# Optimization experiments

Measured on AMD Instinct MI355X. Metric: run time of the kernel, lower is better.

Reference implementation:

```python
import jax, jax.numpy as jnp
import numpy as np

B, L, D, H = 2, 2048, 1024, 16
DH = D // H  # per-head dim = 64


def setup_inputs() -> dict:
    key = jax.random.key(0)
    ks = jax.random.split(key, 7)
    s = 1.0 / np.sqrt(D)
    x = jax.random.normal(ks[0], (B, L, D), dtype=jnp.float32)
    Wq = jax.random.normal(ks[1], (D, D), dtype=jnp.float32) * s
    bq = jax.random.normal(ks[2], (D,), dtype=jnp.float32) * s
    Wk = jax.random.normal(ks[3], (D, D), dtype=jnp.float32) * s
    bk = jax.random.normal(ks[4], (D,), dtype=jnp.float32) * s
    Wv = jax.random.normal(ks[5], (D, D), dtype=jnp.float32) * s
    bv = jax.random.normal(ks[6], (D,), dtype=jnp.float32) * s
    # strict upper-triangular causal mask; mask==1 means position is masked (-inf)
    atten_mask = jnp.triu(jnp.ones((L, L), dtype=jnp.int32), k=1)
    return {"x": x, "atten_mask": atten_mask, "Wq": Wq, "bq": bq,
            "Wk": Wk, "bk": bk, "Wv": Wv, "bv": bv}


def reference(x, atten_mask, Wq, bq, Wk, bk, Wv, bv):
    # nn.Linear: y = x @ W^T + b
    q = x @ Wq.T + bq  # [B,L,D]
    k = x @ Wk.T + bk
    v = x @ Wv.T + bv
    # contiguous split into heads == reshape to [B,L,H,DH]
    q = q.reshape(B, L, H, DH)
    k = k.reshape(B, L, H, DH)
    v = v.reshape(B, L, H, DH)
    scale = jnp.sqrt(jnp.float32(DH))
    scores = jnp.einsum('blhd,bmhd->bhlm', q, k) / scale  # [B,H,L,L]
    # torch.where(mask == 1, -inf, scores)
    scores = jnp.where(atten_mask[None, None] == 1, -jnp.inf, scores)
    attn = jax.nn.softmax(scores, axis=-1)
    out = jnp.einsum('bhlm,bmhd->blhd', attn, v)  # [B,L,H,DH]
    return out.reshape(B, L, D)  # concat heads along channel dim
```

## Files before the change

### kernel.cpp

```cpp
#include <hip/hip_runtime.h>
#include <hip/hip_bf16.h>

#define BDIM 2
#define LSEQ 2048
#define DMODEL 1024
#define NH 16
#define DHEAD 64
#define SP 40
#define RST 68
#define CTS 136

typedef __bf16 bf16_t;
typedef __attribute__((ext_vector_type(8))) __bf16 bf16x8;
typedef __attribute__((ext_vector_type(4))) __bf16 bf16x4;
typedef __attribute__((ext_vector_type(2))) __bf16 bf16x2;
typedef __attribute__((ext_vector_type(4))) float f32x4;
typedef __attribute__((ext_vector_type(4))) int i32x4;

static __device__ __forceinline__ f32x4 mfma16(bf16x8 a, bf16x8 b, f32x4 c) {
    return __builtin_amdgcn_mfma_f32_16x16x32_bf16(a, b, c, 0, 0, 0);
}

static __device__ __forceinline__ void load_lds16(const bf16_t* g, void* l) {
    __builtin_amdgcn_global_load_lds(
        (const __attribute__((address_space(1))) void*)g,
        (__attribute__((address_space(3))) void*)l, 16, 0, 0);
}

__global__ void convert_all(
    const float* __restrict__ x,
    const float* __restrict__ Wq, const float* __restrict__ Wk, const float* __restrict__ Wv,
    const float* __restrict__ bq, const float* __restrict__ bk, const float* __restrict__ bv,
    bf16_t* __restrict__ cx,
    bf16_t* __restrict__ cWq, bf16_t* __restrict__ cWk, bf16_t* __restrict__ cWv,
    bf16_t* __restrict__ cbq, bf16_t* __restrict__ cbk, bf16_t* __restrict__ cbv,
    float SQ)
{
    const int blk = blockIdx.x;
    const float* src; bf16_t* dst; int base, cnt; float sc = 1.0f;
    if (blk < 1024)      { src = x;  dst = cx;  base = blk * 1024;          cnt = 1024; }
    else if (blk < 1280) { src = Wq; dst = cWq; base = (blk - 1024) * 1024; cnt = 1024; sc = SQ; }
    else if (blk < 1536) { src = Wk; dst = cWk; base = (blk - 1280) * 1024; cnt = 1024; }
    else if (blk < 1792) { src = Wv; dst = cWv; base = (blk - 1536) * 1024; cnt = 1024; }
    else if (blk == 1792){ src = bq; dst = cbq; base = 0; cnt = 256; sc = SQ; }
    else if (blk == 1793){ src = bk; dst = cbk; base = 0; cnt = 256; }
    else                 { src = bv; dst = cbv; base = 0; cnt = 256; }

    for (int i = base + threadIdx.x; i < base + cnt; i += 256) {
        f32x4 v = *(const f32x4*)(src + 4 * (size_t)i);
        bf16x4 o;
        o[0] = (bf16_t)(v[0] * sc); o[1] = (bf16_t)(v[1] * sc);
        o[2] = (bf16_t)(v[2] * sc); o[3] = (bf16_t)(v[3] * sc);
        *(bf16x4*)(dst + 4 * (size_t)i) = o;
    }
}

__global__ __launch_bounds__(512, 2) void qkv_gemm(
    const bf16_t* __restrict__ x,
    const bf16_t* __restrict__ W0, const bf16_t* __restrict__ W1, const bf16_t* __restrict__ W2,
    const bf16_t* __restrict__ b0, const bf16_t* __restrict__ b1, const bf16_t* __restrict__ b2,
    bf16_t* __restrict__ yq, bf16_t* __restrict__ yk, bf16_t* __restrict__ yvT)
{
    __shared__ alignas(16) bf16_t smem[81920];

    const int tid  = threadIdx.x;
    const int lane = tid & 63;
    const int w    = tid >> 6;
    const int quad = lane >> 4;
    const int n16  = lane & 15;
    const int swz  = n16 & 7;
    const int srow = lane >> 3;
    const int schnk = (lane & 7) ^ srow;

    const int s   = blockIdx.x;
    const int sem = ((s & 7) << 3) | (s >> 3);
    const int m0  = (sem >> 2) * 256;
    const int n0  = (sem & 3) * 256;
    const int z   = blockIdx.y;

    const bf16_t* W    = (z == 0) ? W0 : ((z == 1) ? W1 : W2);
    const bf16_t* bias = (z == 0) ? b0 : ((z == 1) ? b1 : b2);

    const int wm = (w >> 2) * 128;
    const int wn = (w & 3) * 64;

    const bf16_t* gA = x + (size_t)(m0 + w * 8 + srow) * DMODEL + schnk * 8;
    const bf16_t* gB = W + (size_t)(n0 + w * 8 + srow) * DMODEL + schnk * 8;

    f32x4 acc[8][4] = {};

    auto stageA = [&](int abuf, int h, int kt) {
        bf16_t* d = smem + abuf * 16384 + (h * 128 + w * 8) * 64;
        const bf16_t* src = gA + (size_t)(h * 128) * DMODEL + kt * 64;
        load_lds16(src, d);
        load_lds16(src + (size_t)64 * DMODEL, d + 64 * 64);
    };
    auto stageB = [&](int slot, int h, int kt) {
        bf16_t* d = smem + 32768 + slot * 16384 + (h * 128 + w * 8) * 64;
        const bf16_t* src = gB + (size_t)(h * 128) * DMODEL + kt * 64;
        load_lds16(src, d);
        load_lds16(src + (size_t)64 * DMODEL, d + 64 * 64);
    };

    stageA(0, 0, 0); stageA(0, 1, 0);
    stageB(0, 0, 0); stageB(0, 1, 0);
    stageB(1, 0, 1); stageB(1, 1, 1);
    asm volatile("s_waitcnt vmcnt(4)" ::: "memory");
    __builtin_amdgcn_s_barrier();

    int bs = 0;
    for (int u = 0; u < 16; ++u) {
        const int abuf = u & 1;
        const bf16_t* Ab = smem + abuf * 16384;
        const bf16_t* Bb = smem + 32768 + bs * 16384;
        const int bs2 = (bs + 2 >= 3) ? bs - 1 : bs + 2;

        bf16x8 bfr[4][2], aX[2][2], aY[2][2];

        #pragma unroll
        for (int nt = 0; nt < 4; ++nt) {
            const bf16_t* br = Bb + (wn + nt * 16 + n16) * 64;
            bfr[nt][0] = *(const bf16x8*)(br + ((quad    ) ^ swz) * 8);
            bfr[nt][1] = *(const bf16x8*)(br + ((quad + 4) ^ swz) * 8);
        }
        #pragma unroll
        for (int m2 = 0; m2 < 2; ++m2) {
            const bf16_t* ar = Ab + (wm + m2 * 16 + n16) * 64;
            aX[m2][0] = *(const bf16x8*)(ar + ((quad    ) ^ swz) * 8);
            aX[m2][1] = *(const bf16x8*)(ar + ((quad + 4) ^ swz) * 8);
        }
        if (u + 1 < 16) { stageA(abuf ^ 1, 0, u + 1); stageA(abuf ^ 1, 1, u + 1); }
        if (u + 2 < 16) { stageB(bs2, 0, u + 2);      stageB(bs2, 1, u + 2); }

        #pragma unroll
        for (int m2 = 0; m2 < 2; ++m2) {
            const bf16_t* ar = Ab + (wm + (2 + m2) * 16 + n16) * 64;
            aY[m2][0] = *(const bf16x8*)(ar + ((quad    ) ^ swz) * 8);
            aY[m2][1] = *(const bf16x8*)(ar + ((quad + 4) ^ swz) * 8);
        }
        #pragma unroll
        for (int m2 = 0; m2 < 2; ++m2)
            #pragma unroll
            for (int nt = 0; nt < 4; ++nt) {
                acc[m2][nt] = mfma16(aX[m2][0], bfr[nt][0], acc[m2][nt]);
                acc[m2][nt] = mfma16(aX[m2][1], bfr[nt][1], acc[m2][nt]);
            }

        #pragma unroll
        for (int m2 = 0; m2 < 2; ++m2) {
            const bf16_t* ar = Ab + (wm + (4 + m2) * 16 + n16) * 64;
            aX[m2][0] = *(const bf16x8*)(ar + ((quad    ) ^ swz) * 8);
            aX[m2][1] = *(const bf16x8*)(ar + ((quad + 4) ^ swz) * 8);
        }
        #pragma unroll
        for (int m2 = 0; m2 < 2; ++m2)
            #pragma unroll
            for (int nt = 0; nt < 4; ++nt) {
                acc[2 + m2][nt] = mfma16(aY[m2][0], bfr[nt][0], acc[2 + m2][nt]);
                acc[2 + m2][nt] = mfma16(aY[m2][1], bfr[nt][1], acc[2 + m2][nt]);
            }

        #pragma unroll
        for (int m2 = 0; m2 < 2; ++m2) {
            const bf16_t* ar = Ab + (wm + (6 + m2) * 16 + n16) * 64;
            aY[m2][0] = *(const bf16x8*)(ar + ((quad    ) ^ swz) * 8);
            aY[m2][1] = *(const bf16x8*)(ar + ((quad + 4) ^ swz) * 8);
        }
        #pragma unroll
        for (int m2 = 0; m2 < 2; ++m2)
            #pragma unroll
            for (int nt = 0; nt < 4; ++nt) {
                acc[4 + m2][nt] = mfma16(aX[m2][0], bfr[nt][0], acc[4 + m2][nt]);
                acc[4 + m2][nt] = mfma16(aX[m2][1], bfr[nt][1], acc[4 + m2][nt]);
            }

        #pragma unroll
        for (int m2 = 0; m2 < 2; ++m2)
            #pragma unroll
            for (int nt = 0; nt < 4; ++nt) {
                acc[6 + m2][nt] = mfma16(aY[m2][0], bfr[nt][0], acc[6 + m2][nt]);
                acc[6 + m2][nt] = mfma16(aY[m2][1], bfr[nt][1], acc[6 + m2][nt]);
            }

        if (u < 14) asm volatile("s_waitcnt vmcnt(4)" ::: "memory");
        else        asm volatile("s_waitcnt vmcnt(0)" ::: "memory");
        __builtin_amdgcn_s_barrier();
        bs = (bs + 1 == 3) ? 0 : bs + 1;
    }

    if (z < 2) {
        bf16_t* y = (z == 0) ? yq : yk;
        bf16_t* Ct = smem;
        #pragma unroll
        for (int hp = 0; hp < 2; ++hp) {
            if (((w & 3) >> 1) == hp) {
                #pragma unroll
                for (int nt = 0; nt < 4; ++nt) {
                    const int jc = (w & 1) * 64 + nt * 16 + n16;
                    const float bv = (float)bias[n0 + hp * 128 + jc];
                    #pragma unroll
                    for (int mt = 0; mt < 8; ++mt) {
                        const int rr = wm + mt * 16 + quad * 4;
                        #pragma unroll
                        for (int r = 0; r < 4; ++r)
                            Ct[(rr + r) * CTS + jc] = (bf16_t)(acc[mt][nt][r] + bv);
                    }
                }
            }
            __syncthreads();
            const int row = tid >> 1;
            const int seg = tid & 1;
            const int hh  = (n0 >> 6) + hp * 2 + seg;
            const int i   = m0 + row;
            const int bb  = i >> 11, ll = i & 2047;
            bf16_t* dst = &y[(((size_t)bb * NH + hh) * LSEQ + ll) * DHEAD];
            const bf16_t* srcr = &Ct[row * CTS + seg * 64];
            #pragma unroll
            for (int c = 0; c < 8; ++c)
                *(bf16x8*)(dst + c * 8) = *(const bf16x8*)(srcr + c * 8);
            __syncthreads();
        }
    } else {
        #pragma unroll
        for (int nt = 0; nt < 4; ++nt) {
            const int j = n0 + wn + nt * 16 + n16;
            const float bv = (float)bias[j];
            #pragma unroll
            for (int mt = 0; mt < 8; ++mt) {
                const int i0 = m0 + wm + mt * 16 + quad * 4;
                const int bb = i0 >> 11, l = i0 & 2047;
                bf16x4 pk;
                #pragma unroll
                for (int r = 0; r < 4; ++r) pk[r] = (bf16_t)(acc[mt][nt][r] + bv);
                *(bf16x4*)(&yvT[((size_t)bb * DMODEL + j) * LSEQ + l]) = pk;
            }
        }
    }
}

__global__ __launch_bounds__(256, 2) void attn_fused(
    const bf16_t* __restrict__ qp,
    const bf16_t* __restrict__ kp,
    const bf16_t* __restrict__ vtp,
    float* __restrict__ out,
    float* __restrict__ Opart,
    float* __restrict__ ml)
{
    __shared__ alignas(16) char arena[69632];
    float* Rex = (float*)(arena);

    const int tid  = threadIdx.x;
    const int lane = tid & 63;
    const int w    = tid >> 6;
    const int quad = lane >> 4;
    const int n16  = lane & 15;
    const int lane3 = lane >> 3;
    const int lane7 = lane & 7;
    const int swz8  = (lane7 ^ lane3) * 8;
    const int swz   = n16 & 7;

    const int wq   = (w >> 1) * 64;
    const int wkv  = (w & 1) * 32;
    const int pairI = w >> 1;
    const bool isOdd = (w & 1) != 0;
    bf16_t* Pw0 = (bf16_t*)(arena + 49152) + w * (64 * SP);

    const int bh  = blockIdx.x;
    const int yy  = blockIdx.y;
    const int p   = yy & 7;
    const bool isA = (yy < 8);
    const int b = bh >> 4, h = bh & 15;
    const size_t hb = (size_t)bh * (LSEQ * DHEAD);

    float l_[4];
    f32x4 oacc[4][4];

    auto zero_state = [&]() {
        #pragma unroll
        for (int g = 0; g < 4; ++g) {
            l_[g] = 0.f;
            #pragma unroll
            for (int mv = 0; mv < 4; ++mv) { f32x4 zz = {0.f,0.f,0.f,0.f}; oacc[mv][g] = zz; }
        }
    };

    auto process = [&](int qt, int t0, int ntiles, bool maskTail) {
        int iqg[4];
        bf16x8 qb[4][2];
        #pragma unroll
        for (int g = 0; g < 4; ++g) {
            iqg[g] = qt * 128 + wq + 16 * g + n16;
            const bf16_t* qq = qp + hb + (size_t)iqg[g] * DHEAD;
            qb[g][0] = *(const bf16x8*)(qq + quad * 8);
            qb[g][1] = *(const bf16x8*)(qq + 32 + quad * 8);
        }

        const bf16_t* gk0 = kp  + hb + (size_t)(t0 * 64 + 16 * w + lane3) * DHEAD + swz8;
        const bf16_t* gv0 = vtp + hb + (size_t)(16 * w + lane3) * LSEQ + t0 * 64 + swz8;

        auto stageKV = [&](int slot, int it) {
            char* lk = arena + slot * 8192 + w * 2048;
            char* lv = arena + 24576 + slot * 8192 + w * 2048;
            const bf16_t* kK = gk0 + (size_t)it * 64 * DHEAD;
            const bf16_t* vV = gv0 + (size_t)it * 64;
            load_lds16(kK,             lk);
            load_lds16(kK + 8 * DHEAD, lk + 1024);
            load_lds16(vV,             lv);
            load_lds16(vV + 8 * LSEQ,  lv + 1024);
        };

        stageKV(0, 0);
        if (ntiles > 1) { stageKV(1, 1); asm volatile("s_waitcnt vmcnt(4)" ::: "memory"); }
        else            {                asm volatile("s_waitcnt vmcnt(0)" ::: "memory"); }
        __builtin_amdgcn_s_barrier();

        int slot = 0;
        for (int it = 0; it < ntiles; ++it) {
            const int s2 = (slot + 2 >= 3) ? slot - 1 : slot + 2;
            if (it + 2 < ntiles) stageKV(s2, it + 2);

            const bf16_t* kb = (const bf16_t*)(arena + slot * 8192);
            f32x4 s[2][4];
            #pragma unroll
            for (int m = 0; m < 2; ++m) {
                const bf16_t* krow = kb + (wkv + 16 * m + n16) * 64;
                bf16x8 k0v = *(const bf16x8*)(krow + ((quad    ) ^ swz) * 8);
                bf16x8 k1v = *(const bf16x8*)(krow + ((quad + 4) ^ swz) * 8);
                #pragma unroll
                for (int g = 0; g < 4; ++g) {
                    f32x4 z = {0.f, 0.f, 0.f, 0.f};
                    z = mfma16(k0v, qb[g][0], z);
                    z = mfma16(k1v, qb[g][1], z);
                    s[m][g] = z;
                }
            }

            if (maskTail && it >= ntiles - 2) {
                const int k0 = (t0 + it) * 64 + wkv;
                #pragma unroll
                for (int m = 0; m < 2; ++m)
                    #pragma unroll
                    for (int g = 0; g < 4; ++g)
                        #pragma unroll
                        for (int r = 0; r < 4; ++r)
                            if (k0 + 16 * m + quad * 4 + r > iqg[g]) s[m][g][r] = -1e30f;
            }

            #pragma unroll
            for (int g = 0; g < 4; ++g) {
                float rs = 0.f;
                #pragma unroll
                for (int m = 0; m < 2; ++m) {
                    float p0 = __builtin_amdgcn_exp2f(s[m][g][0]);
                    float p1 = __builtin_amdgcn_exp2f(s[m][g][1]);
                    float p2 = __builtin_amdgcn_exp2f(s[m][g][2]);
                    float p3 = __builtin_amdgcn_exp2f(s[m][g][3]);
                    rs += (p0 + p1) + (p2 + p3);
                    bf16x4 pk;
                    pk[0] = (bf16_t)p0; pk[1] = (bf16_t)p1;
                    pk[2] = (bf16_t)p2; pk[3] = (bf16_t)p3;
                    *(bf16x4*)(Pw0 + (16 * g + n16) * SP + 16 * m + quad * 4) = pk;
                }
                l_[g] += rs;
            }

            asm volatile("s_waitcnt lgkmcnt(0)" ::: "memory");

            const bf16_t* vb = (const bf16_t*)(arena + 24576 + slot * 8192);
            bf16x8 pb[4];
            #pragma unroll
            for (int g = 0; g < 4; ++g)
                pb[g] = *(const bf16x8*)(Pw0 + (16 * g + n16) * SP + quad * 8);
            #pragma unroll
            for (int mv = 0; mv < 4; ++mv) {
                const bf16_t* vrow = vb + (16 * mv + n16) * 64;
                bf16x8 va = *(const bf16x8*)(vrow + ((((w & 1) * 4) + quad) ^ swz) * 8);
                #pragma unroll
                for (int g = 0; g < 4; ++g)
                    oacc[mv][g] = mfma16(va, pb[g], oacc[mv][g]);
            }

            if (it + 2 < ntiles) asm volatile("s_waitcnt vmcnt(4)" ::: "memory");
            else                 asm volatile("s_waitcnt vmcnt(0)" ::: "memory");
            __builtin_amdgcn_s_barrier();
            slot = (slot + 1 == 3) ? 0 : slot + 1;
        }
    };

    auto reduce_pair = [&]() {
        __syncthreads();
        float* Rb = Rex + pairI * (64 * RST);
        if (isOdd) {
            #pragma unroll
            for (int g = 0; g < 4; ++g) {
                #pragma unroll
                for (int mv = 0; mv < 4; ++mv)
                    *(f32x4*)(Rb + (16 * g + n16) * RST + 16 * mv + quad * 4) = oacc[mv][g];
                Rb[(16 * g + n16) * RST + 64 + quad] = l_[g];
            }
        }
        __syncthreads();
        if (!isOdd) {
            #pragma unroll
            for (int g = 0; g < 4; ++g) {
                #pragma unroll
                for (int mv = 0; mv < 4; ++mv) {
                    f32x4 t = *(const f32x4*)(Rb + (16 * g + n16) * RST + 16 * mv + quad * 4);
                    oacc[mv][g][0] += t[0]; oacc[mv][g][1] += t[1];
                    oacc[mv][g][2] += t[2]; oacc[mv][g][3] += t[3];
                }
                float ls = l_[g] + Rb[(16 * g + n16) * RST + 64 + quad];
                ls += __shfl_xor(ls, 16, 64);
                ls += __shfl_xor(ls, 32, 64);
                l_[g] = ls;
            }
        }
        __syncthreads();
    };

    auto store_partial = [&](int pidx) {
        if (isOdd) return;
        #pragma unroll
        for (int g = 0; g < 4; ++g) {
            const int row = wq + 16 * g + n16;
            float* Ob = Opart + (size_t)pidx * (128 * 64) + row * 64;
            #pragma unroll
            for (int mv = 0; mv < 4; ++mv)
                *(f32x4*)(Ob + 16 * mv + quad * 4) = oacc[mv][g];
            if (quad == 0) ml[(size_t)pidx * 128 + row] = l_[g];
        }
    };

    if (isA) {
        zero_state();
        process(p, 0, 2 * p + 2, true);
        reduce_pair();
        if (!isOdd) {
            #pragma unroll
            for (int g = 0; g < 4; ++g) {
                const float inv = 1.0f / l_[g];
                const int iq = p * 128 + wq + 16 * g + n16;
                float* orow = out + ((size_t)b * LSEQ + iq) * DMODEL + h * DHEAD;
                #pragma unroll
                for (int mv = 0; mv < 4; ++mv) {
                    f32x4 o;
                    o[0] = oacc[mv][g][0] * inv; o[1] = oacc[mv][g][1] * inv;
                    o[2] = oacc[mv][g][2] * inv; o[3] = oacc[mv][g][3] * inv;
                    *(f32x4*)(orow + 16 * mv + quad * 4) = o;
                }
            }
        }
        zero_state();
        process(15 - p, 0, 15 - 2 * p, false);
        reduce_pair();
        store_partial((bh * 8 + (7 - p)) * 2 + 0);
    } else {
        zero_state();
        process(15 - p, 15 - 2 * p, 17, true);
        reduce_pair();
        store_partial((bh * 8 + (7 - p)) * 2 + 1);
    }
}

__global__ __launch_bounds__(256) void attn_combine(
    const float* __restrict__ Opart, const float* __restrict__ ml,
    float* __restrict__ out)
{
    const int bh = blockIdx.x;
    const int q8 = blockIdx.y;
    const int t  = threadIdx.x;
    const int row = t >> 1;
    const int dh0 = (t & 1) * 32;
    const int p0  = (bh * 8 + q8) * 2;
    const int b = bh >> 4, h = bh & 15;

    float l0 = ml[(size_t)p0 * 128 + row];
    float l1 = ml[(size_t)(p0 + 1) * 128 + row];
    float inv = 1.0f / (l0 + l1);

    const float* P0 = Opart + (size_t)p0 * (128 * 64) + row * 64 + dh0;
    const float* P1 = P0 + 128 * 64;
    float* orow = out + ((size_t)b * LSEQ + ((8 + q8) * 128 + row)) * DMODEL
                + h * DHEAD + dh0;
    #pragma unroll
    for (int c = 0; c < 8; ++c) {
        f32x4 o0 = *(const f32x4*)(P0 + 4 * c);
        f32x4 o1 = *(const f32x4*)(P1 + 4 * c);
        f32x4 o;
        o[0] = (o0[0] + o1[0]) * inv;
        o[1] = (o0[1] + o1[1]) * inv;
        o[2] = (o0[2] + o1[2]) * inv;
        o[3] = (o0[3] + o1[3]) * inv;
        *(f32x4*)(orow + 4 * c) = o;
    }
}

extern "C" void kernel_launch(void* const* d_in, const int* in_sizes, int n_in,
                              void* d_out, int out_size, void* d_ws, size_t ws_size,
                              hipStream_t stream)
{
    const float* x  = (const float*)d_in[0];
    const float* Wq = (const float*)d_in[2];
    const float* bq = (const float*)d_in[3];
    const float* Wk = (const float*)d_in[4];
    const float* bk = (const float*)d_in[5];
    const float* Wv = (const float*)d_in[6];
    const float* bv = (const float*)d_in[7];
    float* out = (float*)d_out;

    char* ws = (char*)d_ws;
    bf16_t* q   = (bf16_t*)(ws);
    bf16_t* k   = (bf16_t*)(ws + 8u  * 1024 * 1024);
    bf16_t* vT  = (bf16_t*)(ws + 16u * 1024 * 1024);
    bf16_t* cx  = (bf16_t*)(ws + 24u * 1024 * 1024);
    bf16_t* cWq = (bf16_t*)(ws + 32u * 1024 * 1024);
    bf16_t* cWk = (bf16_t*)(ws + 34u * 1024 * 1024);
    bf16_t* cWv = (bf16_t*)(ws + 36u * 1024 * 1024);
    bf16_t* cbq = (bf16_t*)(ws + 38u * 1024 * 1024);
    bf16_t* cbk = (bf16_t*)(ws + 38u * 1024 * 1024 + 4096);
    bf16_t* cbv = (bf16_t*)(ws + 38u * 1024 * 1024 + 8192);
    float*  mlp = (float*) (ws + 39u * 1024 * 1024);
    float*  Op  = (float*) (ws + 40u * 1024 * 1024);

    const float SQ = 0.125f * 1.44269504088896f;

    convert_all<<<1795, 256, 0, stream>>>(x, Wq, Wk, Wv, bq, bk, bv,
                                          cx, cWq, cWk, cWv, cbq, cbk, cbv, SQ);

    dim3 g1(64, 3, 1);
    qkv_gemm<<<g1, 512, 0, stream>>>(cx, cWq, cWk, cWv, cbq, cbk, cbv, q, k, vT);

    dim3 g2(BDIM * NH, 16, 1);
    attn_fused<<<g2, 256, 0, stream>>>(q, k, vT, out, Op, mlp);

    dim3 g3(BDIM * NH, 8, 1);
    attn_combine<<<g3, 256, 0, stream>>>(Op, mlp, out);
}
```

Before: 167.3 us.

## Shrink QKV GEMM to 128x128 tiles with simple double-buffered pipeline

Replaces the 256x256 tile, 512-thread QKV projection GEMM (triple-buffered B, double-buffered A, interleaved fragment loads, swizzled block order) with a 128x128 tile, 256-thread kernel using plain double buffering and __syncthreads. The grid grows from 192 to 768 blocks, which improves occupancy and load balance across CUs. In exchange, operand reuse per block drops and global/L2 traffic rises. The finer-grained prefetch/barrier scheduling is also lost.

Measured after the change: 168.9 us. No clear change (+0.9%).

```diff
diff --git a/kernel.cpp b/kernel.cpp
--- a/kernel.cpp
+++ b/kernel.cpp
@@ -55,180 +55,125 @@
     }
 }
 
-__global__ __launch_bounds__(512, 2) void qkv_gemm(
+__global__ __launch_bounds__(256) void qkv_gemm(
     const bf16_t* __restrict__ x,
     const bf16_t* __restrict__ W0, const bf16_t* __restrict__ W1, const bf16_t* __restrict__ W2,
     const bf16_t* __restrict__ b0, const bf16_t* __restrict__ b1, const bf16_t* __restrict__ b2,
     bf16_t* __restrict__ yq, bf16_t* __restrict__ yk, bf16_t* __restrict__ yvT)
 {
-    __shared__ alignas(16) bf16_t smem[81920];
+    __shared__ alignas(16) bf16_t smem[2 * 16384];
+    bf16_t* Ct = smem;
 
     const int tid  = threadIdx.x;
     const int lane = tid & 63;
     const int w    = tid >> 6;
     const int quad = lane >> 4;
     const int n16  = lane & 15;
-    const int swz  = n16 & 7;
-    const int srow = lane >> 3;
-    const int schnk = (lane & 7) ^ srow;
-
-    const int s   = blockIdx.x;
-    const int sem = ((s & 7) << 3) | (s >> 3);
-    const int m0  = (sem >> 2) * 256;
-    const int n0  = (sem & 3) * 256;
-    const int z   = blockIdx.y;
+
+    const int m0 = blockIdx.y * 128;
+    const int n0 = blockIdx.x * 128;
+    const int z  = blockIdx.z;
 
     const bf16_t* W    = (z == 0) ? W0 : ((z == 1) ? W1 : W2);
     const bf16_t* bias = (z == 0) ? b0 : ((z == 1) ? b1 : b2);
 
-    const int wm = (w >> 2) * 128;
-    const int wn = (w & 3) * 64;
-
-    const bf16_t* gA = x + (size_t)(m0 + w * 8 + srow) * DMODEL + schnk * 8;
-    const bf16_t* gB = W + (size_t)(n0 + w * 8 + srow) * DMODEL + schnk * 8;
-
-    f32x4 acc[8][4] = {};
-
-    auto stageA = [&](int abuf, int h, int kt) {
-        bf16_t* d = smem + abuf * 16384 + (h * 128 + w * 8) * 64;
-        const bf16_t* src = gA + (size_t)(h * 128) * DMODEL + kt * 64;
-        load_lds16(src, d);
-        load_lds16(src + (size_t)64 * DMODEL, d + 64 * 64);
-    };
-    auto stageB = [&](int slot, int h, int kt) {
-        bf16_t* d = smem + 32768 + slot * 16384 + (h * 128 + w * 8) * 64;
-        const bf16_t* src = gB + (size_t)(h * 128) * DMODEL + kt * 64;
-        load_lds16(src, d);
-        load_lds16(src + (size_t)64 * DMODEL, d + 64 * 64);
-    };
-
-    stageA(0, 0, 0); stageA(0, 1, 0);
-    stageB(0, 0, 0); stageB(0, 1, 0);
-    stageB(1, 0, 1); stageB(1, 1, 1);
-    asm volatile("s_waitcnt vmcnt(4)" ::: "memory");
-    __builtin_amdgcn_s_barrier();
-
-    int bs = 0;
-    for (int u = 0; u < 16; ++u) {
-        const int abuf = u & 1;
-        const bf16_t* Ab = smem + abuf * 16384;
-        const bf16_t* Bb = smem + 32768 + bs * 16384;
-        const int bs2 = (bs + 2 >= 3) ? bs - 1 : bs + 2;
-
-        bf16x8 bfr[4][2], aX[2][2], aY[2][2];
-
-        #pragma unroll
-        for (int nt = 0; nt < 4; ++nt) {
-            const bf16_t* br = Bb + (wn + nt * 16 + n16) * 64;
-            bfr[nt][0] = *(const bf16x8*)(br + ((quad    ) ^ swz) * 8);
-            bfr[nt][1] = *(const bf16x8*)(br + ((quad + 4) ^ swz) * 8);
-        }
-        #pragma unroll
-        for (int m2 = 0; m2 < 2; ++m2) {
-            const bf16_t* ar = Ab + (wm + m2 * 16 + n16) * 64;
-            aX[m2][0] = *(const bf16x8*)(ar + ((quad    ) ^ swz) * 8);
-            aX[m2][1] = *(const bf16x8*)(ar + ((quad + 4) ^ swz) * 8);
-        }
-        if (u + 1 < 16) { stageA(abuf ^ 1, 0, u + 1); stageA(abuf ^ 1, 1, u + 1); }
-        if (u + 2 < 16) { stageB(bs2, 0, u + 2);      stageB(bs2, 1, u + 2); }
-
-        #pragma unroll
-        for (int m2 = 0; m2 < 2; ++m2) {
-            const bf16_t* ar = Ab + (wm + (2 + m2) * 16 + n16) * 64;
-            aY[m2][0] = *(const bf16x8*)(ar + ((quad    ) ^ swz) * 8);
-            aY[m2][1] = *(const bf16x8*)(ar + ((quad + 4) ^ swz) * 8);
-        }
-        #pragma unroll
-        for (int m2 = 0; m2 < 2; ++m2)
+    const int wm = (w >> 1) * 64;
+    const int wn = (w & 1) * 64;
+
+    f32x4 acc[4][4] = {};
+
+    const int srow  = lane >> 3;
+    const int schnk = (lane & 7) ^ srow;
+    const bf16_t* gx = x + (size_t)(m0 + w * 32 + srow) * DMODEL + schnk * 8;
+    const bf16_t* gw = W + (size_t)(n0 + w * 32 + srow) * DMODEL + schnk * 8;
+    const int dOff = w * 2048;
+
+    const int swz = n16 & 7;
+
+    {
+        bf16_t* lA = smem + dOff;
+        bf16_t* lB = smem + 8192 + dOff;
+        #pragma unroll
+        for (int ii = 0; ii < 4; ++ii) {
+            load_lds16(gx + (size_t)(8 * ii) * DMODEL, lA + ii * 512);
+            load_lds16(gw + (size_t)(8 * ii) * DMODEL, lB + ii * 512);
+        }
+    }
+    __syncthreads();
+
+    int buf = 0;
+    for (int it = 0; it < 16; ++it) {
+        if (it + 1 < 16) {
+            const int k0 = (it + 1) * 64;
+            bf16_t* lA = smem + (buf ^ 1) * 16384 + dOff;
+            bf16_t* lB = smem + (buf ^ 1) * 16384 + 8192 + dOff;
+            #pragma unroll
+            for (int ii = 0; ii < 4; ++ii) {
+                load_lds16(gx + (size_t)(8 * ii) * DMODEL + k0, lA + ii * 512);
+                load_lds16(gw + (size_t)(8 * ii) * DMODEL + k0, lB + ii * 512);
+            }
+        }
+
+        const bf16_t* Ab = smem + buf * 16384;
+        const bf16_t* Bb = smem + buf * 16384 + 8192;
+        #pragma unroll
+        for (int kk = 0; kk < 2; ++kk) {
+            bf16x8 af[4], bfv[4];
+            #pragma unroll
+            for (int mt = 0; mt < 4; ++mt) {
+                const bf16_t* ar = Ab + (wm + mt * 16 + n16) * 64;
+                af[mt] = *(const bf16x8*)(ar + ((quad + 4 * kk) ^ swz) * 8);
+            }
             #pragma unroll
             for (int nt = 0; nt < 4; ++nt) {
-                acc[m2][nt] = mfma16(aX[m2][0], bfr[nt][0], acc[m2][nt]);
-                acc[m2][nt] = mfma16(aX[m2][1], bfr[nt][1], acc[m2][nt]);
-            }
-
-        #pragma unroll
-        for (int m2 = 0; m2 < 2; ++m2) {
-            const bf16_t* ar = Ab + (wm + (4 + m2) * 16 + n16) * 64;
-            aX[m2][0] = *(const bf16x8*)(ar + ((quad    ) ^ swz) * 8);
-            aX[m2][1] = *(const bf16x8*)(ar + ((quad + 4) ^ swz) * 8);
-        }
-        #pragma unroll
-        for (int m2 = 0; m2 < 2; ++m2)
-            #pragma unroll
-            for (int nt = 0; nt < 4; ++nt) {
-                acc[2 + m2][nt] = mfma16(aY[m2][0], bfr[nt][0], acc[2 + m2][nt]);
-                acc[2 + m2][nt] = mfma16(aY[m2][1], bfr[nt][1], acc[2 + m2][nt]);
-            }
-
-        #pragma unroll
-        for (int m2 = 0; m2 < 2; ++m2) {
-            const bf16_t* ar = Ab + (wm + (6 + m2) * 16 + n16) * 64;
-            aY[m2][0] = *(const bf16x8*)(ar + ((quad    ) ^ swz) * 8);
-            aY[m2][1] = *(const bf16x8*)(ar + ((quad + 4) ^ swz) * 8);
-        }
-        #pragma unroll
-        for (int m2 = 0; m2 < 2; ++m2)
-            #pragma unroll
-            for (int nt = 0; nt < 4; ++nt) {
-                acc[4 + m2][nt] = mfma16(aX[m2][0], bfr[nt][0], acc[4 + m2][nt]);
-                acc[4 + m2][nt] = mfma16(aX[m2][1], bfr[nt][1], acc[4 + m2][nt]);
-            }
-
-        #pragma unroll
-        for (int m2 = 0; m2 < 2; ++m2)
-            #pragma unroll
-            for (int nt = 0; nt < 4; ++nt) {
-                acc[6 + m2][nt] = mfma16(aY[m2][0], bfr[nt][0], acc[6 + m2][nt]);
-                acc[6 + m2][nt] = mfma16(aY[m2][1], bfr[nt][1], acc[6 + m2][nt]);
-            }
-
-        if (u < 14) asm volatile("s_waitcnt vmcnt(4)" ::: "memory");
-        else        asm volatile("s_waitcnt vmcnt(0)" ::: "memory");
-        __builtin_amdgcn_s_barrier();
-        bs = (bs + 1 == 3) ? 0 : bs + 1;
+                const bf16_t* br = Bb + (wn + nt * 16 + n16) * 64;
+                bfv[nt] = *(const bf16x8*)(br + ((quad + 4 * kk) ^ swz) * 8);
+            }
+            #pragma unroll
+            for (int mt = 0; mt < 4; ++mt)
+                #pragma unroll
+                for (int nt = 0; nt < 4; ++nt)
+                    acc[mt][nt] = mfma16(af[mt], bfv[nt], acc[mt][nt]);
+        }
+
+        __syncthreads();
+        buf ^= 1;
     }
 
     if (z < 2) {
         bf16_t* y = (z == 0) ? yq : yk;
-        bf16_t* Ct = smem;
-        #pragma unroll
-        for (int hp = 0; hp < 2; ++hp) {
-            if (((w & 3) >> 1) == hp) {
-                #pragma unroll
-                for (int nt = 0; nt < 4; ++nt) {
-                    const int jc = (w & 1) * 64 + nt * 16 + n16;
-                    const float bv = (float)bias[n0 + hp * 128 + jc];
-                    #pragma unroll
-                    for (int mt = 0; mt < 8; ++mt) {
-                        const int rr = wm + mt * 16 + quad * 4;
-                        #pragma unroll
-                        for (int r = 0; r < 4; ++r)
-                            Ct[(rr + r) * CTS + jc] = (bf16_t)(acc[mt][nt][r] + bv);
-                    }
-                }
-            }
-            __syncthreads();
-            const int row = tid >> 1;
-            const int seg = tid & 1;
-            const int hh  = (n0 >> 6) + hp * 2 + seg;
-            const int i   = m0 + row;
-            const int bb  = i >> 11, ll = i & 2047;
-            bf16_t* dst = &y[(((size_t)bb * NH + hh) * LSEQ + ll) * DHEAD];
-            const bf16_t* srcr = &Ct[row * CTS + seg * 64];
-            #pragma unroll
-            for (int c = 0; c < 8; ++c)
-                *(bf16x8*)(dst + c * 8) = *(const bf16x8*)(srcr + c * 8);
-            __syncthreads();
-        }
+        #pragma unroll
+        for (int nt = 0; nt < 4; ++nt) {
+            int jc = wn + nt * 16 + n16;
+            float bv = (float)bias[n0 + jc];
+            #pragma unroll
+            for (int mt = 0; mt < 4; ++mt) {
+                int rr = wm + mt * 16 + quad * 4;
+                #pragma unroll
+                for (int r = 0; r < 4; ++r)
+                    Ct[(rr + r) * CTS + jc] = (bf16_t)(acc[mt][nt][r] + bv);
+            }
+        }
+        __syncthreads();
+        const int l    = tid >> 1;
+        const int half = tid & 1;
+        const int hh   = (n0 >> 6) + half;
+        const int i    = m0 + l;
+        const int bb   = i >> 11, ll = i & 2047;
+        bf16_t* dst = &y[(((size_t)bb * NH + hh) * LSEQ + ll) * DHEAD];
+        const bf16_t* srcr = &Ct[l * CTS + half * 64];
+        #pragma unroll
+        for (int c = 0; c < 8; ++c)
+            *(bf16x8*)(dst + c * 8) = *(const bf16x8*)(srcr + c * 8);
     } else {
         #pragma unroll
         for (int nt = 0; nt < 4; ++nt) {
-            const int j = n0 + wn + nt * 16 + n16;
-            const float bv = (float)bias[j];
-            #pragma unroll
-            for (int mt = 0; mt < 8; ++mt) {
-                const int i0 = m0 + wm + mt * 16 + quad * 4;
-                const int bb = i0 >> 11, l = i0 & 2047;
+            int j = n0 + wn + nt * 16 + n16;
+            float bv = (float)bias[j];
+            #pragma unroll
+            for (int mt = 0; mt < 4; ++mt) {
+                int i0 = m0 + wm + mt * 16 + quad * 4;
+                int bb = i0 >> 11, l = i0 & 2047;
                 bf16x4 pk;
                 #pragma unroll
                 for (int r = 0; r < 4; ++r) pk[r] = (bf16_t)(acc[mt][nt][r] + bv);
@@ -527,8 +472,8 @@
     convert_all<<<1795, 256, 0, stream>>>(x, Wq, Wk, Wv, bq, bk, bv,
                                           cx, cWq, cWk, cWv, cbq, cbk, cbv, SQ);
 
-    dim3 g1(64, 3, 1);
-    qkv_gemm<<<g1, 512, 0, stream>>>(cx, cWq, cWk, cWv, cbq, cbk, cbv, q, k, vT);
+    dim3 g1(DMODEL / 128, (BDIM * LSEQ) / 128, 3);
+    qkv_gemm<<<g1, 256, 0, stream>>>(cx, cWq, cWk, cWv, cbq, cbk, cbv, q, k, vT);
 
     dim3 g2(BDIM * NH, 16, 1);
     attn_fused<<<g2, 256, 0, stream>>>(q, k, vT, out, Op, mlp);
```
